# Optimization experiments

Measured on AMD Instinct MI355X. Metric: run time of the kernel, lower is better.

## Reference

```python
import jax, jax.numpy as jnp
import numpy as np

N_NODES = 20000
N_EDGES = 320000
DIN, DMID, DOUT, HEADS = 256, 256, 64, 8
NEG_SLOPE = 0.2  # PyG GATv2Conv default negative_slope


def _gatv2_layer(x, src, dst, n, Wl, bl, Wr, br, att, bias, concat):
    """One GATv2Conv layer (inference: attention dropout disabled).
    x: [N, din]; src/dst: [E] (self-loops already included);
    Wl/Wr: [din, H*D]; bl/br: [H*D]; att: [H, D]; bias: [H*D] or [D].
    """
    H, D = att.shape
    xl = (x @ Wl + bl).reshape(-1, H, D)   # source-side transform
    xr = (x @ Wr + br).reshape(-1, H, D)   # target-side transform
    m = xl[src] + xr[dst]                  # [E, H, D]
    e = jnp.sum(jax.nn.leaky_relu(m, NEG_SLOPE) * att, axis=-1)  # [E, H]
    # segment softmax over edges sharing a destination node
    emax = jax.ops.segment_max(e, dst, num_segments=n)           # [N, H]
    p = jnp.exp(e - emax[dst])
    denom = jax.ops.segment_sum(p, dst, num_segments=n)          # [N, H]
    alpha = p / denom[dst]                                       # [E, H]
    out = jax.ops.segment_sum(alpha[:, :, None] * xl[src], dst, num_segments=n)  # [N, H, D]
    out = out.reshape(n, H * D) if concat else out.mean(axis=1)
    return out + bias


def _forward(x, edge_index,
             Wl0, bl0, Wr0, br0, att0, bias0,
             Wl1, bl1, Wr1, br1, att1, bias1,
             Wl2, bl2, Wr2, br2, att2, bias2):
    n = x.shape[0]
    loops = jnp.arange(n, dtype=edge_index.dtype)  # PyG add_self_loops=True
    src = jnp.concatenate([edge_index[0], loops])
    dst = jnp.concatenate([edge_index[1], loops])
    # feature dropout is identity at inference
    h = jax.nn.elu(_gatv2_layer(x, src, dst, n, Wl0, bl0, Wr0, br0, att0, bias0, True))
    prev_h = jnp.zeros_like(h)
    h_in = h + prev_h
    h = jax.nn.elu(_gatv2_layer(h_in, src, dst, n, Wl1, bl1, Wr1, br1, att1, bias1, True))
    prev_h = h_in
    h_in = h + prev_h
    out = _gatv2_layer(h_in, src, dst, n, Wl2, bl2, Wr2, br2, att2, bias2, False)
    return out


def setup_inputs() -> dict:
    key = jax.random.key(0)
    ks = jax.random.split(key, 20)
    Dh_mid = DMID // HEADS  # 32
    def lin(k, din, dout):
        return jax.random.normal(k, (din, dout), jnp.float32) * (1.0 / np.sqrt(din))
    inp = {
        "x": jax.random.normal(ks[0], (N_NODES, DIN), jnp.float32),
        "edge_index": jax.random.randint(ks[1], (2, N_EDGES), 0, N_NODES, jnp.int32),
        # layer 0: GATv2Conv(256, 32, heads=8, concat=True)
        "Wl0": lin(ks[2], DIN, HEADS * Dh_mid), "bl0": jnp.zeros((HEADS * Dh_mid,), jnp.float32),
        "Wr0": lin(ks[3], DIN, HEADS * Dh_mid), "br0": jnp.zeros((HEADS * Dh_mid,), jnp.float32),
        "att0": jax.random.normal(ks[4], (HEADS, Dh_mid), jnp.float32) * 0.1,
        "bias0": jnp.zeros((HEADS * Dh_mid,), jnp.float32),
        # layer 1: GATv2Conv(256, 32, heads=8, concat=True)
        "Wl1": lin(ks[5], DMID, HEADS * Dh_mid), "bl1": jnp.zeros((HEADS * Dh_mid,), jnp.float32),
        "Wr1": lin(ks[6], DMID, HEADS * Dh_mid), "br1": jnp.zeros((HEADS * Dh_mid,), jnp.float32),
        "att1": jax.random.normal(ks[7], (HEADS, Dh_mid), jnp.float32) * 0.1,
        "bias1": jnp.zeros((HEADS * Dh_mid,), jnp.float32),
        # layer 2: GATv2Conv(256, 64, heads=8, concat=False)
        "Wl2": lin(ks[8], DMID, HEADS * DOUT), "bl2": jnp.zeros((HEADS * DOUT,), jnp.float32),
        "Wr2": lin(ks[9], DMID, HEADS * DOUT), "br2": jnp.zeros((HEADS * DOUT,), jnp.float32),
        "att2": jax.random.normal(ks[10], (HEADS, DOUT), jnp.float32) * 0.1,
        "bias2": jnp.zeros((DOUT,), jnp.float32),
    }
    return inp


def reference(x, edge_index,
              Wl0, bl0, Wr0, br0, att0, bias0,
              Wl1, bl1, Wr1, br1, att1, bias1,
              Wl2, bl2, Wr2, br2, att2, bias2):
    return _forward(x, edge_index,
                    Wl0, bl0, Wr0, br0, att0, bias0,
                    Wl1, bl1, Wr1, br1, att1, bias1,
                    Wl2, bl2, Wr2, br2, att2, bias2)
```

## Files before the change

### kernel.cpp

```cpp
#include <hip/hip_runtime.h>
#include <math.h>


#define DIN   256
#define NNODE_K 256

typedef __attribute__((ext_vector_type(8))) short short8v;
typedef __attribute__((ext_vector_type(4))) float floatx4;

static __device__ __forceinline__ unsigned short f2bf(float f) {
    unsigned int u = __float_as_uint(f);
    unsigned int r = (u + 0x7FFFu + ((u >> 16) & 1u)) >> 16;
    return (unsigned short)r;
}
static __device__ __forceinline__ float bf2f(unsigned short h) {
    return __uint_as_float(((unsigned int)h) << 16);
}
static __device__ __forceinline__ float lrelu(float m) {
    return m > 0.f ? m : 0.2f * m;
}


__global__ void k_init_cnt(int* cnt, int n) {
    int i = blockIdx.x * blockDim.x + threadIdx.x;
    if (i < n) cnt[i] = 1;
}

__global__ void k_count(const int* __restrict__ ei, int* cnt, int E) {
    int e = blockIdx.x * blockDim.x + threadIdx.x;
    if (e < E) atomicAdd(&cnt[ei[E + e]], 1);
}

__global__ void k_scan(const int* __restrict__ cnt, int* __restrict__ row_ptr, int n) {
    __shared__ int sm[256];
    int tid = threadIdx.x;
    int carry = 0;
    if (tid == 0) row_ptr[0] = 0;
    for (int base = 0; base < n; base += 256) {
        int i = base + tid;
        int v = (i < n) ? cnt[i] : 0;
        sm[tid] = v;
        __syncthreads();
        for (int off = 1; off < 256; off <<= 1) {
            int t = (tid >= off) ? sm[tid - off] : 0;
            __syncthreads();
            sm[tid] += t;
            __syncthreads();
        }
        if (i < n) row_ptr[i + 1] = carry + sm[tid];
        carry += sm[255];
        __syncthreads();
    }
}

__global__ void k_selfloop(const int* __restrict__ row_ptr, int* __restrict__ csr_src,
                           int* __restrict__ cnt, int n) {
    int v = blockIdx.x * blockDim.x + threadIdx.x;
    if (v < n) {
        csr_src[row_ptr[v]] = v;
        cnt[v] = 1;
    }
}

__global__ void k_scatter(const int* __restrict__ ei, const int* __restrict__ row_ptr,
                          int* __restrict__ cnt, int* __restrict__ csr_src, int E) {
    int e = blockIdx.x * blockDim.x + threadIdx.x;
    if (e < E) {
        int d = ei[E + e];
        int pos = row_ptr[d] + atomicAdd(&cnt[d], 1);
        csr_src[pos] = ei[e];
    }
}


__global__ __launch_bounds__(256) void k_split(const float* __restrict__ X,
                                               unsigned short* __restrict__ Xh,
                                               unsigned short* __restrict__ Xl,
                                               int total4) {
    int i = blockIdx.x * blockDim.x + threadIdx.x;
    if (i >= total4) return;
    float4 f = ((const float4*)X)[i];
    ushort4 h, l;
    h.x = f2bf(f.x); l.x = f2bf(f.x - bf2f(h.x));
    h.y = f2bf(f.y); l.y = f2bf(f.y - bf2f(h.y));
    h.z = f2bf(f.z); l.z = f2bf(f.z - bf2f(h.z));
    h.w = f2bf(f.w); l.w = f2bf(f.w - bf2f(h.w));
    ((ushort4*)Xh)[i] = h;
    ((ushort4*)Xl)[i] = l;
}


__global__ __launch_bounds__(256) void k_wsplit(const float* __restrict__ W,
                                                unsigned short* __restrict__ WhT,
                                                unsigned short* __restrict__ WlT,
                                                int N) {
    __shared__ float t[64][65];
    int kb = blockIdx.x * 64, nb = blockIdx.y * 64;
    int tid = threadIdx.x;
    int c = tid & 63, r4 = tid >> 6;
    #pragma unroll
    for (int it = 0; it < 16; ++it) {
        int r = it * 4 + r4;
        t[r][c] = W[(size_t)(kb + r) * N + nb + c];
    }
    __syncthreads();
    #pragma unroll
    for (int it = 0; it < 16; ++it) {
        int n = it * 4 + r4;
        int k = c;
        float f = t[k][n];
        unsigned short hi = f2bf(f);
        unsigned short lo = f2bf(f - bf2f(hi));
        WhT[(size_t)(nb + n) * NNODE_K + kb + k] = hi;
        WlT[(size_t)(nb + n) * NNODE_K + kb + k] = lo;
    }
}


#define GBM 128
#define GBN 128
#define GBK 64

__global__ __launch_bounds__(256) void gemm_mfma(
    const unsigned short* __restrict__ Ah, const unsigned short* __restrict__ Al,
    const unsigned short* __restrict__ WhT, const unsigned short* __restrict__ WlT,
    const float* __restrict__ bias, float* __restrict__ C, int M, int N) {
    __shared__ char smem[GBM * GBK * 2 * 2];
    char* sA = smem;
    char* sB = smem + GBM * GBK * 2;
    int tid = threadIdx.x;
    int lane = tid & 63, wid = tid >> 6;
    int wr = wid >> 1, wc = wid & 1;
    int row0 = blockIdx.y * GBM, col0 = blockIdx.x * GBN;

    floatx4 acc[4][4];
    #pragma unroll
    for (int m = 0; m < 4; ++m)
        #pragma unroll
        for (int n = 0; n < 4; ++n)
            acc[m][n] = (floatx4){0.f, 0.f, 0.f, 0.f};

    const unsigned short* Asrc[3] = {Ah, Al, Ah};
    const unsigned short* Bsrc[3] = {WhT, WhT, WlT};

    for (int t = 0; t < 3; ++t) {
        const unsigned short* Ap = Asrc[t];
        const unsigned short* Bp = Bsrc[t];
        for (int k0 = 0; k0 < NNODE_K; k0 += GBK) {
            #pragma unroll
            for (int it = 0; it < 4; ++it) {
                int c = it * 256 + tid;
                int row = c >> 3, slot = c & 7;
                int sl = slot ^ (row & 7);
                int gr = row0 + row; if (gr >= M) gr = M - 1;
                *(int4*)(sA + c * 16) =
                    *(const int4*)(Ap + (size_t)gr * NNODE_K + k0 + sl * 8);
                *(int4*)(sB + c * 16) =
                    *(const int4*)(Bp + (size_t)(col0 + row) * NNODE_K + k0 + sl * 8);
            }
            __syncthreads();
            #pragma unroll
            for (int kk = 0; kk < 2; ++kk) {
                short8v a[4], b[4];
                #pragma unroll
                for (int m = 0; m < 4; ++m) {
                    int ra = wr * 64 + m * 16 + (lane & 15);
                    int st = (kk * 4 + (lane >> 4)) ^ (ra & 7);
                    a[m] = *(const short8v*)(sA + ra * 128 + st * 16);
                }
                #pragma unroll
                for (int n = 0; n < 4; ++n) {
                    int rb = wc * 64 + n * 16 + (lane & 15);
                    int st = (kk * 4 + (lane >> 4)) ^ (rb & 7);
                    b[n] = *(const short8v*)(sB + rb * 128 + st * 16);
                }
                #pragma unroll
                for (int m = 0; m < 4; ++m)
                    #pragma unroll
                    for (int n = 0; n < 4; ++n)
                        acc[m][n] = __builtin_amdgcn_mfma_f32_16x16x32_bf16(
                            a[m], b[n], acc[m][n], 0, 0, 0);
            }
            __syncthreads();
        }
    }

    #pragma unroll
    for (int n = 0; n < 4; ++n) {
        int col = col0 + wc * 64 + n * 16 + (lane & 15);
        float bv = bias[col];
        #pragma unroll
        for (int m = 0; m < 4; ++m) {
            int rbase = row0 + wr * 64 + m * 16 + (lane >> 4) * 4;
            #pragma unroll
            for (int r = 0; r < 4; ++r) {
                int row = rbase + r;
                if (row < M) C[(size_t)row * N + col] = acc[m][n][r] + bv;
            }
        }
    }
}


template<int MODE>
__global__ __launch_bounds__(256) void gat_agg_mid(
    const float* __restrict__ xl, const float* __restrict__ xr,
    const float* __restrict__ att, const int* __restrict__ row_ptr,
    const int* __restrict__ csr_src, const float* __restrict__ bias,
    unsigned short* __restrict__ Sh, unsigned short* __restrict__ Sl, int n) {
    int wid = threadIdx.x >> 6, lane = threadIdx.x & 63;
    int v = blockIdx.x * 4 + wid;
    if (v >= n) return;
    int idx = 4 * lane;
    float4 xrv  = *(const float4*)(xr + (size_t)v * 256 + idx);
    float4 attv = *(const float4*)(att + idx);
    float4 acc = make_float4(0.f, 0.f, 0.f, 0.f);
    float lsum = 0.f, mval = -INFINITY;

    int e0 = row_ptr[v], e1 = row_ptr[v + 1];
    for (int base = e0; base < e1; base += 8) {
        int cnt = e1 - base; if (cnt > 8) cnt = 8;
        int s[8];
        float4 xv[8];
        #pragma unroll
        for (int j = 0; j < 8; ++j) {
            int ee = base + j;
            s[j] = csr_src[ee < e1 ? ee : base];
        }
        #pragma unroll
        for (int j = 0; j < 8; ++j)
            xv[j] = *(const float4*)(xl + (size_t)s[j] * 256 + idx);
        #pragma unroll
        for (int j = 0; j < 8; ++j) {
            if (j >= cnt) break;
            float p = lrelu(xv[j].x + xrv.x) * attv.x + lrelu(xv[j].y + xrv.y) * attv.y +
                      lrelu(xv[j].z + xrv.z) * attv.z + lrelu(xv[j].w + xrv.w) * attv.w;
            p += __shfl_xor(p, 1); p += __shfl_xor(p, 2); p += __shfl_xor(p, 4);
            if (p > mval) {
                float sc = __expf(mval - p);
                acc.x *= sc; acc.y *= sc; acc.z *= sc; acc.w *= sc;
                lsum *= sc; mval = p;
            }
            float pe = __expf(p - mval);
            lsum += pe;
            acc.x += pe * xv[j].x; acc.y += pe * xv[j].y;
            acc.z += pe * xv[j].z; acc.w += pe * xv[j].w;
        }
    }

    float inv = 1.f / lsum;
    float4 bb = *(const float4*)(bias + idx);
    float o[4] = {acc.x * inv + bb.x, acc.y * inv + bb.y,
                  acc.z * inv + bb.z, acc.w * inv + bb.w};
    #pragma unroll
    for (int j = 0; j < 4; ++j) o[j] = o[j] > 0.f ? o[j] : (__expf(o[j]) - 1.f);
    if (MODE == 1) {
        ushort4 rh = *(const ushort4*)(Sh + (size_t)v * 256 + idx);
        ushort4 rl = *(const ushort4*)(Sl + (size_t)v * 256 + idx);
        o[0] += bf2f(rh.x) + bf2f(rl.x);
        o[1] += bf2f(rh.y) + bf2f(rl.y);
        o[2] += bf2f(rh.z) + bf2f(rl.z);
        o[3] += bf2f(rh.w) + bf2f(rl.w);
    }
    ushort4 hi, lo;
    hi.x = f2bf(o[0]); lo.x = f2bf(o[0] - bf2f(hi.x));
    hi.y = f2bf(o[1]); lo.y = f2bf(o[1] - bf2f(hi.y));
    hi.z = f2bf(o[2]); lo.z = f2bf(o[2] - bf2f(hi.z));
    hi.w = f2bf(o[3]); lo.w = f2bf(o[3] - bf2f(hi.w));
    *(ushort4*)(Sh + (size_t)v * 256 + idx) = hi;
    *(ushort4*)(Sl + (size_t)v * 256 + idx) = lo;
}


__global__ __launch_bounds__(256) void gat_agg_out(
    const float* __restrict__ xl, const float* __restrict__ xr,
    const float* __restrict__ att, const int* __restrict__ row_ptr,
    const int* __restrict__ csr_src, const float* __restrict__ bias,
    float* __restrict__ out, int n) {
    int wid = threadIdx.x >> 6, lane = threadIdx.x & 63;
    int v = blockIdx.x * 4 + wid;
    if (v >= n) return;
    int idx = 4 * lane;
    float4 xr0 = *(const float4*)(xr + (size_t)v * 512 + idx);
    float4 xr1 = *(const float4*)(xr + (size_t)v * 512 + 256 + idx);
    float4 at0 = *(const float4*)(att + idx);
    float4 at1 = *(const float4*)(att + 256 + idx);
    float4 a0 = make_float4(0.f, 0.f, 0.f, 0.f), a1 = a0;
    float ls0 = 0.f, ls1 = 0.f, m0 = -INFINITY, m1 = -INFINITY;

    int e0 = row_ptr[v], e1 = row_ptr[v + 1];
    for (int base = e0; base < e1; base += 4) {
        int cnt = e1 - base; if (cnt > 4) cnt = 4;
        int s[4];
        float4 x0[4], x1[4];
        #pragma unroll
        for (int j = 0; j < 4; ++j) {
            int ee = base + j;
            s[j] = csr_src[ee < e1 ? ee : base];
        }
        #pragma unroll
        for (int j = 0; j < 4; ++j) {
            x0[j] = *(const float4*)(xl + (size_t)s[j] * 512 + idx);
            x1[j] = *(const float4*)(xl + (size_t)s[j] * 512 + 256 + idx);
        }
        #pragma unroll
        for (int j = 0; j < 4; ++j) {
            if (j >= cnt) break;
            float p0 = lrelu(x0[j].x + xr0.x) * at0.x + lrelu(x0[j].y + xr0.y) * at0.y +
                       lrelu(x0[j].z + xr0.z) * at0.z + lrelu(x0[j].w + xr0.w) * at0.w;
            float p1 = lrelu(x1[j].x + xr1.x) * at1.x + lrelu(x1[j].y + xr1.y) * at1.y +
                       lrelu(x1[j].z + xr1.z) * at1.z + lrelu(x1[j].w + xr1.w) * at1.w;
            #pragma unroll
            for (int msk = 1; msk < 16; msk <<= 1) {
                p0 += __shfl_xor(p0, msk);
                p1 += __shfl_xor(p1, msk);
            }
            if (p0 > m0) {
                float sc = __expf(m0 - p0);
                a0.x *= sc; a0.y *= sc; a0.z *= sc; a0.w *= sc; ls0 *= sc; m0 = p0;
            }
            float pe0 = __expf(p0 - m0);
            ls0 += pe0;
            a0.x += pe0 * x0[j].x; a0.y += pe0 * x0[j].y;
            a0.z += pe0 * x0[j].z; a0.w += pe0 * x0[j].w;
            if (p1 > m1) {
                float sc = __expf(m1 - p1);
                a1.x *= sc; a1.y *= sc; a1.z *= sc; a1.w *= sc; ls1 *= sc; m1 = p1;
            }
            float pe1 = __expf(p1 - m1);
            ls1 += pe1;
            a1.x += pe1 * x1[j].x; a1.y += pe1 * x1[j].y;
            a1.z += pe1 * x1[j].z; a1.w += pe1 * x1[j].w;
        }
    }

    float i0 = 1.f / ls0, i1 = 1.f / ls1;
    float o[4] = {a0.x * i0 + a1.x * i1, a0.y * i0 + a1.y * i1,
                  a0.z * i0 + a1.z * i1, a0.w * i0 + a1.w * i1};
    #pragma unroll
    for (int j = 0; j < 4; ++j) {
        o[j] += __shfl_xor(o[j], 16);
        o[j] += __shfl_xor(o[j], 32);
    }
    if (lane < 16) {
        float4 bb = *(const float4*)(bias + idx);
        float4 res;
        res.x = o[0] * 0.125f + bb.x;
        res.y = o[1] * 0.125f + bb.y;
        res.z = o[2] * 0.125f + bb.z;
        res.w = o[3] * 0.125f + bb.w;
        *(float4*)(out + (size_t)v * 64 + idx) = res;
    }
}


extern "C" void kernel_launch(void* const* d_in, const int* in_sizes, int n_in,
                              void* d_out, int out_size, void* d_ws, size_t ws_size,
                              hipStream_t stream) {
    const float* x     = (const float*)d_in[0];
    const int*   ei    = (const int*)  d_in[1];
    const float* Wl0   = (const float*)d_in[2];
    const float* bl0   = (const float*)d_in[3];
    const float* Wr0   = (const float*)d_in[4];
    const float* br0   = (const float*)d_in[5];
    const float* att0  = (const float*)d_in[6];
    const float* bias0 = (const float*)d_in[7];
    const float* Wl1   = (const float*)d_in[8];
    const float* bl1   = (const float*)d_in[9];
    const float* Wr1   = (const float*)d_in[10];
    const float* br1   = (const float*)d_in[11];
    const float* att1  = (const float*)d_in[12];
    const float* bias1 = (const float*)d_in[13];
    const float* Wl2   = (const float*)d_in[14];
    const float* bl2   = (const float*)d_in[15];
    const float* Wr2   = (const float*)d_in[16];
    const float* br2   = (const float*)d_in[17];
    const float* att2  = (const float*)d_in[18];
    const float* bias2 = (const float*)d_in[19];

    const int N = in_sizes[0] / DIN;
    const int E = in_sizes[1] / 2;

    char* ws = (char*)d_ws;
    size_t off = 0;
    auto carve = [&](size_t bytes) {
        void* p = ws + off;
        off = (off + bytes + 15) & ~(size_t)15;
        return p;
    };
    int*            row_ptr = (int*)           carve((size_t)(N + 1) * 4);
    int*            cnt     = (int*)           carve((size_t)N * 4);
    int*            csr_src = (int*)           carve((size_t)(E + N) * 4);
    float*          xl      = (float*)         carve((size_t)N * 512 * 4);
    float*          xr      = (float*)         carve((size_t)N * 512 * 4);
    unsigned short* Ah      = (unsigned short*)carve((size_t)N * 256 * 2);
    unsigned short* Al      = (unsigned short*)carve((size_t)N * 256 * 2);
    unsigned short* WhT     = (unsigned short*)carve((size_t)512 * 256 * 2);
    unsigned short* WlT     = (unsigned short*)carve((size_t)512 * 256 * 2);

    float* outp = (float*)d_out;

    k_init_cnt<<<(N + 255) / 256, 256, 0, stream>>>(cnt, N);
    k_count   <<<(E + 255) / 256, 256, 0, stream>>>(ei, cnt, E);
    k_scan    <<<1, 256, 0, stream>>>(cnt, row_ptr, N);
    k_selfloop<<<(N + 255) / 256, 256, 0, stream>>>(row_ptr, csr_src, cnt, N);
    k_scatter <<<(E + 255) / 256, 256, 0, stream>>>(ei, row_ptr, cnt, csr_src, E);

    dim3 blk(256);
    const int aggGrid = (N + 3) / 4;
    dim3 gemmGrid256(2, (N + GBM - 1) / GBM);
    dim3 gemmGrid512(4, (N + GBM - 1) / GBM);
    dim3 wsGrid256(4, 4), wsGrid512(4, 8);

    k_split<<<(N * 256 / 4 + 255) / 256, blk, 0, stream>>>(x, Ah, Al, N * 256 / 4);

    k_wsplit<<<wsGrid256, blk, 0, stream>>>(Wl0, WhT, WlT, 256);
    gemm_mfma<<<gemmGrid256, blk, 0, stream>>>(Ah, Al, WhT, WlT, bl0, xl, N, 256);
    k_wsplit<<<wsGrid256, blk, 0, stream>>>(Wr0, WhT, WlT, 256);
    gemm_mfma<<<gemmGrid256, blk, 0, stream>>>(Ah, Al, WhT, WlT, br0, xr, N, 256);
    gat_agg_mid<0><<<aggGrid, blk, 0, stream>>>(
        xl, xr, att0, row_ptr, csr_src, bias0, Ah, Al, N);

    k_wsplit<<<wsGrid256, blk, 0, stream>>>(Wl1, WhT, WlT, 256);
    gemm_mfma<<<gemmGrid256, blk, 0, stream>>>(Ah, Al, WhT, WlT, bl1, xl, N, 256);
    k_wsplit<<<wsGrid256, blk, 0, stream>>>(Wr1, WhT, WlT, 256);
    gemm_mfma<<<gemmGrid256, blk, 0, stream>>>(Ah, Al, WhT, WlT, br1, xr, N, 256);
    gat_agg_mid<1><<<aggGrid, blk, 0, stream>>>(
        xl, xr, att1, row_ptr, csr_src, bias1, Ah, Al, N);

    k_wsplit<<<wsGrid512, blk, 0, stream>>>(Wl2, WhT, WlT, 512);
    gemm_mfma<<<gemmGrid512, blk, 0, stream>>>(Ah, Al, WhT, WlT, bl2, xl, N, 512);
    k_wsplit<<<wsGrid512, blk, 0, stream>>>(Wr2, WhT, WlT, 512);
    gemm_mfma<<<gemmGrid512, blk, 0, stream>>>(Ah, Al, WhT, WlT, br2, xr, N, 512);
    gat_agg_out<<<aggGrid, blk, 0, stream>>>(
        xl, xr, att2, row_ptr, csr_src, bias2, outp, N);
}
```

Measured before the change: 656.9 us.

## Fuse Wl/Wr GEMMs, parallelize scan, use direct-to-LDS loads, widen output batching

Concatenates the left and right weight matrices so each layer does one GEMM producing an interleaved [N, 2*HD] xl|xr buffer, halving GEMM and weight-split launches. Replaces the single-block serial scan with a three-kernel block scan. GEMM tile loads now use global_load_lds to write straight into LDS instead of going through registers. The output aggregation batches 8 neighbors per iteration instead of 4. The interleaved layout doubles the row stride for the gathers, and the larger batch raises register pressure.

```diff
diff --git a/kernel.cpp b/kernel.cpp
--- a/kernel.cpp
+++ b/kernel.cpp
@@ -7,6 +7,13 @@
 
 typedef __attribute__((ext_vector_type(8))) short short8v;
 typedef __attribute__((ext_vector_type(4))) float floatx4;
+
+typedef __attribute__((address_space(1))) void gas_t;
+typedef __attribute__((address_space(3))) void las_t;
+static __device__ __forceinline__ void gload_lds16(const void* g, void* l) {
+    __builtin_amdgcn_global_load_lds((gas_t*)(uintptr_t)g, (las_t*)(uintptr_t)l,
+                                     16, 0, 0);
+}
 
 static __device__ __forceinline__ unsigned short f2bf(float f) {
     unsigned int u = __float_as_uint(f);
@@ -31,26 +38,45 @@
     if (e < E) atomicAdd(&cnt[ei[E + e]], 1);
 }
 
-__global__ void k_scan(const int* __restrict__ cnt, int* __restrict__ row_ptr, int n) {
+__global__ __launch_bounds__(256) void k_scan_blocks(
+    const int* __restrict__ cnt, int* __restrict__ row_ptr,
+    int* __restrict__ bsum, int n) {
     __shared__ int sm[256];
     int tid = threadIdx.x;
-    int carry = 0;
-    if (tid == 0) row_ptr[0] = 0;
-    for (int base = 0; base < n; base += 256) {
-        int i = base + tid;
-        int v = (i < n) ? cnt[i] : 0;
-        sm[tid] = v;
+    int i = blockIdx.x * 256 + tid;
+    int v = (i < n) ? cnt[i] : 0;
+    sm[tid] = v;
+    __syncthreads();
+    for (int off = 1; off < 256; off <<= 1) {
+        int t = (tid >= off) ? sm[tid - off] : 0;
         __syncthreads();
-        for (int off = 1; off < 256; off <<= 1) {
-            int t = (tid >= off) ? sm[tid - off] : 0;
-            __syncthreads();
-            sm[tid] += t;
-            __syncthreads();
-        }
-        if (i < n) row_ptr[i + 1] = carry + sm[tid];
-        carry += sm[255];
+        sm[tid] += t;
         __syncthreads();
     }
+    if (i < n) row_ptr[i + 1] = sm[tid];
+    if (tid == 255) bsum[blockIdx.x] = sm[255];
+}
+
+__global__ __launch_bounds__(256) void k_scan_tops(int* bsum, int nb) {
+    __shared__ int sm[256];
+    int tid = threadIdx.x;
+    int v = (tid < nb) ? bsum[tid] : 0;
+    sm[tid] = v;
+    __syncthreads();
+    for (int off = 1; off < 256; off <<= 1) {
+        int t = (tid >= off) ? sm[tid - off] : 0;
+        __syncthreads();
+        sm[tid] += t;
+        __syncthreads();
+    }
+    if (tid < nb) bsum[tid] = sm[tid] - v;
+}
+
+__global__ void k_scan_add(int* __restrict__ row_ptr,
+                           const int* __restrict__ bsum, int n) {
+    int i = blockIdx.x * 256 + threadIdx.x;
+    if (i < n) row_ptr[i + 1] += bsum[blockIdx.x];
+    if (i == 0) row_ptr[0] = 0;
 }
 
 __global__ void k_selfloop(const int* __restrict__ row_ptr, int* __restrict__ csr_src,
@@ -90,18 +116,20 @@
 }
 
 
-__global__ __launch_bounds__(256) void k_wsplit(const float* __restrict__ W,
-                                                unsigned short* __restrict__ WhT,
-                                                unsigned short* __restrict__ WlT,
-                                                int N) {
+__global__ __launch_bounds__(256) void k_wsplit2(
+    const float* __restrict__ Wl, const float* __restrict__ Wr,
+    unsigned short* __restrict__ WhT, unsigned short* __restrict__ WlT, int Nh) {
     __shared__ float t[64][65];
-    int kb = blockIdx.x * 64, nb = blockIdx.y * 64;
+    int kb = blockIdx.x * 64;
+    int nbg = blockIdx.y * 64;
+    const float* W = (nbg < Nh) ? Wl : Wr;
+    int nb = (nbg < Nh) ? nbg : nbg - Nh;
     int tid = threadIdx.x;
     int c = tid & 63, r4 = tid >> 6;
     #pragma unroll
     for (int it = 0; it < 16; ++it) {
         int r = it * 4 + r4;
-        t[r][c] = W[(size_t)(kb + r) * N + nb + c];
+        t[r][c] = W[(size_t)(kb + r) * Nh + nb + c];
     }
     __syncthreads();
     #pragma unroll
@@ -111,8 +139,8 @@
         float f = t[k][n];
         unsigned short hi = f2bf(f);
         unsigned short lo = f2bf(f - bf2f(hi));
-        WhT[(size_t)(nb + n) * NNODE_K + kb + k] = hi;
-        WlT[(size_t)(nb + n) * NNODE_K + kb + k] = lo;
+        WhT[(size_t)(nbg + n) * NNODE_K + kb + k] = hi;
+        WlT[(size_t)(nbg + n) * NNODE_K + kb + k] = lo;
     }
 }
 
@@ -124,7 +152,8 @@
 __global__ __launch_bounds__(256) void gemm_mfma(
     const unsigned short* __restrict__ Ah, const unsigned short* __restrict__ Al,
     const unsigned short* __restrict__ WhT, const unsigned short* __restrict__ WlT,
-    const float* __restrict__ bias, float* __restrict__ C, int M, int N) {
+    const float* __restrict__ bl, const float* __restrict__ br, int HN,
+    float* __restrict__ C, int M, int N) {
     __shared__ char smem[GBM * GBK * 2 * 2];
     char* sA = smem;
     char* sB = smem + GBM * GBK * 2;
@@ -153,10 +182,10 @@
                 int row = c >> 3, slot = c & 7;
                 int sl = slot ^ (row & 7);
                 int gr = row0 + row; if (gr >= M) gr = M - 1;
-                *(int4*)(sA + c * 16) =
-                    *(const int4*)(Ap + (size_t)gr * NNODE_K + k0 + sl * 8);
-                *(int4*)(sB + c * 16) =
-                    *(const int4*)(Bp + (size_t)(col0 + row) * NNODE_K + k0 + sl * 8);
+                char* dA = sA + (it * 256 + wid * 64) * 16;
+                char* dB = sB + (it * 256 + wid * 64) * 16;
+                gload_lds16(Ap + (size_t)gr * NNODE_K + k0 + sl * 8, dA);
+                gload_lds16(Bp + (size_t)(col0 + row) * NNODE_K + k0 + sl * 8, dB);
             }
             __syncthreads();
             #pragma unroll
@@ -188,7 +217,7 @@
     #pragma unroll
     for (int n = 0; n < 4; ++n) {
         int col = col0 + wc * 64 + n * 16 + (lane & 15);
-        float bv = bias[col];
+        float bv = (col < HN) ? bl[col] : br[col - HN];
         #pragma unroll
         for (int m = 0; m < 4; ++m) {
             int rbase = row0 + wr * 64 + m * 16 + (lane >> 4) * 4;
@@ -204,15 +233,15 @@
 
 template<int MODE>
 __global__ __launch_bounds__(256) void gat_agg_mid(
-    const float* __restrict__ xl, const float* __restrict__ xr,
-    const float* __restrict__ att, const int* __restrict__ row_ptr,
-    const int* __restrict__ csr_src, const float* __restrict__ bias,
+    const float* __restrict__ xlr, const float* __restrict__ att,
+    const int* __restrict__ row_ptr, const int* __restrict__ csr_src,
+    const float* __restrict__ bias,
     unsigned short* __restrict__ Sh, unsigned short* __restrict__ Sl, int n) {
     int wid = threadIdx.x >> 6, lane = threadIdx.x & 63;
     int v = blockIdx.x * 4 + wid;
     if (v >= n) return;
     int idx = 4 * lane;
-    float4 xrv  = *(const float4*)(xr + (size_t)v * 256 + idx);
+    float4 xrv  = *(const float4*)(xlr + (size_t)v * 512 + 256 + idx);
     float4 attv = *(const float4*)(att + idx);
     float4 acc = make_float4(0.f, 0.f, 0.f, 0.f);
     float lsum = 0.f, mval = -INFINITY;
@@ -229,7 +258,7 @@
         }
         #pragma unroll
         for (int j = 0; j < 8; ++j)
-            xv[j] = *(const float4*)(xl + (size_t)s[j] * 256 + idx);
+            xv[j] = *(const float4*)(xlr + (size_t)s[j] * 512 + idx);
         #pragma unroll
         for (int j = 0; j < 8; ++j) {
             if (j >= cnt) break;
@@ -273,38 +302,37 @@
 
 
 __global__ __launch_bounds__(256) void gat_agg_out(
-    const float* __restrict__ xl, const float* __restrict__ xr,
-    const float* __restrict__ att, const int* __restrict__ row_ptr,
-    const int* __restrict__ csr_src, const float* __restrict__ bias,
-    float* __restrict__ out, int n) {
+    const float* __restrict__ xlr, const float* __restrict__ att,
+    const int* __restrict__ row_ptr, const int* __restrict__ csr_src,
+    const float* __restrict__ bias, float* __restrict__ out, int n) {
     int wid = threadIdx.x >> 6, lane = threadIdx.x & 63;
     int v = blockIdx.x * 4 + wid;
     if (v >= n) return;
     int idx = 4 * lane;
-    float4 xr0 = *(const float4*)(xr + (size_t)v * 512 + idx);
-    float4 xr1 = *(const float4*)(xr + (size_t)v * 512 + 256 + idx);
+    float4 xr0 = *(const float4*)(xlr + (size_t)v * 1024 + 512 + idx);
+    float4 xr1 = *(const float4*)(xlr + (size_t)v * 1024 + 768 + idx);
     float4 at0 = *(const float4*)(att + idx);
     float4 at1 = *(const float4*)(att + 256 + idx);
     float4 a0 = make_float4(0.f, 0.f, 0.f, 0.f), a1 = a0;
     float ls0 = 0.f, ls1 = 0.f, m0 = -INFINITY, m1 = -INFINITY;
 
     int e0 = row_ptr[v], e1 = row_ptr[v + 1];
-    for (int base = e0; base < e1; base += 4) {
-        int cnt = e1 - base; if (cnt > 4) cnt = 4;
-        int s[4];
-        float4 x0[4], x1[4];
-        #pragma unroll
-        for (int j = 0; j < 4; ++j) {
+    for (int base = e0; base < e1; base += 8) {
+        int cnt = e1 - base; if (cnt > 8) cnt = 8;
+        int s[8];
+        float4 x0[8], x1[8];
+        #pragma unroll
+        for (int j = 0; j < 8; ++j) {
             int ee = base + j;
             s[j] = csr_src[ee < e1 ? ee : base];
         }
         #pragma unroll
-        for (int j = 0; j < 4; ++j) {
-            x0[j] = *(const float4*)(xl + (size_t)s[j] * 512 + idx);
-            x1[j] = *(const float4*)(xl + (size_t)s[j] * 512 + 256 + idx);
-        }
-        #pragma unroll
-        for (int j = 0; j < 4; ++j) {
+        for (int j = 0; j < 8; ++j) {
+            x0[j] = *(const float4*)(xlr + (size_t)s[j] * 1024 + idx);
+            x1[j] = *(const float4*)(xlr + (size_t)s[j] * 1024 + 256 + idx);
+        }
+        #pragma unroll
+        for (int j = 0; j < 8; ++j) {
             if (j >= cnt) break;
             float p0 = lrelu(x0[j].x + xr0.x) * at0.x + lrelu(x0[j].y + xr0.y) * at0.y +
                        lrelu(x0[j].z + xr0.z) * at0.z + lrelu(x0[j].w + xr0.w) * at0.w;
@@ -380,6 +408,7 @@
 
     const int N = in_sizes[0] / DIN;
     const int E = in_sizes[1] / 2;
+    const int NB = (N + 255) / 256;
 
     char* ws = (char*)d_ws;
     size_t off = 0;
@@ -390,48 +419,47 @@
     };
     int*            row_ptr = (int*)           carve((size_t)(N + 1) * 4);
     int*            cnt     = (int*)           carve((size_t)N * 4);
+    int*            bsum    = (int*)           carve((size_t)256 * 4);
     int*            csr_src = (int*)           carve((size_t)(E + N) * 4);
-    float*          xl      = (float*)         carve((size_t)N * 512 * 4);
-    float*          xr      = (float*)         carve((size_t)N * 512 * 4);
+    float*          xlr     = (float*)         carve((size_t)N * 1024 * 4);
     unsigned short* Ah      = (unsigned short*)carve((size_t)N * 256 * 2);
     unsigned short* Al      = (unsigned short*)carve((size_t)N * 256 * 2);
-    unsigned short* WhT     = (unsigned short*)carve((size_t)512 * 256 * 2);
-    unsigned short* WlT     = (unsigned short*)carve((size_t)512 * 256 * 2);
+    unsigned short* WhT     = (unsigned short*)carve((size_t)1024 * 256 * 2);
+    unsigned short* WlT     = (unsigned short*)carve((size_t)1024 * 256 * 2);
 
     float* outp = (float*)d_out;
 
-    k_init_cnt<<<(N + 255) / 256, 256, 0, stream>>>(cnt, N);
-    k_count   <<<(E + 255) / 256, 256, 0, stream>>>(ei, cnt, E);
-    k_scan    <<<1, 256, 0, stream>>>(cnt, row_ptr, N);
-    k_selfloop<<<(N + 255) / 256, 256, 0, stream>>>(row_ptr, csr_src, cnt, N);
-    k_scatter <<<(E + 255) / 256, 256, 0, stream>>>(ei, row_ptr, cnt, csr_src, E);
+    k_init_cnt   <<<NB, 256, 0, stream>>>(cnt, N);
+    k_count      <<<(E + 255) / 256, 256, 0, stream>>>(ei, cnt, E);
+    k_scan_blocks<<<NB, 256, 0, stream>>>(cnt, row_ptr, bsum, N);
+    k_scan_tops  <<<1, 256, 0, stream>>>(bsum, NB);
+    k_scan_add   <<<NB, 256, 0, stream>>>(row_ptr, bsum, N);
+    k_selfloop   <<<NB, 256, 0, stream>>>(row_ptr, csr_src, cnt, N);
+    k_scatter    <<<(E + 255) / 256, 256, 0, stream>>>(ei, row_ptr, cnt, csr_src, E);
 
     dim3 blk(256);
     const int aggGrid = (N + 3) / 4;
-    dim3 gemmGrid256(2, (N + GBM - 1) / GBM);
     dim3 gemmGrid512(4, (N + GBM - 1) / GBM);
-    dim3 wsGrid256(4, 4), wsGrid512(4, 8);
+    dim3 gemmGrid1024(8, (N + GBM - 1) / GBM);
+    dim3 wsGrid512(4, 8), wsGrid1024(4, 16);
 
     k_split<<<(N * 256 / 4 + 255) / 256, blk, 0, stream>>>(x, Ah, Al, N * 256 / 4);
 
-    k_wsplit<<<wsGrid256, blk, 0, stream>>>(Wl0, WhT, WlT, 256);
-    gemm_mfma<<<gemmGrid256, blk, 0, stream>>>(Ah, Al, WhT, WlT, bl0, xl, N, 256);
-    k_wsplit<<<wsGrid256, blk, 0, stream>>>(Wr0, WhT, WlT, 256);
-    gemm_mfma<<<gemmGrid256, blk, 0, stream>>>(Ah, Al, WhT, WlT, br0, xr, N, 256);
+    k_wsplit2<<<wsGrid512, blk, 0, stream>>>(Wl0, Wr0, WhT, WlT, 256);
+    gemm_mfma<<<gemmGrid512, blk, 0, stream>>>(Ah, Al, WhT, WlT, bl0, br0, 256,
+                                               xlr, N, 512);
     gat_agg_mid<0><<<aggGrid, blk, 0, stream>>>(
-        xl, xr, att0, row_ptr, csr_src, bias0, Ah, Al, N);
-
-    k_wsplit<<<wsGrid256, blk, 0, stream>>>(Wl1, WhT, WlT, 256);
-    gemm_mfma<<<gemmGrid256, blk, 0, stream>>>(Ah, Al, WhT, WlT, bl1, xl, N, 256);
-    k_wsplit<<<wsGrid256, blk, 0, stream>>>(Wr1, WhT, WlT, 256);
-    gemm_mfma<<<gemmGrid256, blk, 0, stream>>>(Ah, Al, WhT, WlT, br1, xr, N, 256);
+        xlr, att0, row_ptr, csr_src, bias0, Ah, Al, N);
+
+    k_wsplit2<<<wsGrid512, blk, 0, stream>>>(Wl1, Wr1, WhT, WlT, 256);
+    gemm_mfma<<<gemmGrid512, blk, 0, stream>>>(Ah, Al, WhT, WlT, bl1, br1, 256,
+                                               xlr, N, 512);
     gat_agg_mid<1><<<aggGrid, blk, 0, stream>>>(
-        xl, xr, att1, row_ptr, csr_src, bias1, Ah, Al, N);
-
-    k_wsplit<<<wsGrid512, blk, 0, stream>>>(Wl2, WhT, WlT, 512);
-    gemm_mfma<<<gemmGrid512, blk, 0, stream>>>(Ah, Al, WhT, WlT, bl2, xl, N, 512);
-    k_wsplit<<<wsGrid512, blk, 0, stream>>>(Wr2, WhT, WlT, 512);
-    gemm_mfma<<<gemmGrid512, blk, 0, stream>>>(Ah, Al, WhT, WlT, br2, xr, N, 512);
+        xlr, att1, row_ptr, csr_src, bias1, Ah, Al, N);
+
+    k_wsplit2<<<wsGrid1024, blk, 0, stream>>>(Wl2, Wr2, WhT, WlT, 512);
+    gemm_mfma<<<gemmGrid1024, blk, 0, stream>>>(Ah, Al, WhT, WlT, bl2, br2, 512,
+                                                xlr, N, 1024);
     gat_agg_out<<<aggGrid, blk, 0, stream>>>(
-        xl, xr, att2, row_ptr, csr_src, bias2, outp, N);
-}
+        xlr, att2, row_ptr, csr_src, bias2, outp, N);
+}
```

Result: faster. 565.6 us (-13.9%).
